# Kernel tuning notes

Hardware: AMD Instinct MI355X
Metric: run time of the kernel (lower is better)

The kernel has to match this reference:

```python
import jax, jax.numpy as jnp
import numpy as np

INF = jnp.inf

def _pairwise_dist(x, y):
    # torch.cdist(x, y, p=2): Euclidean distance matrix [B, N, M]
    x2 = jnp.sum(x * x, axis=-1)  # [B, N]
    y2 = jnp.sum(y * y, axis=-1)  # [B, M]
    sq = x2[:, :, None] + y2[:, None, :] - 2.0 * jnp.einsum('bnf,bmf->bnm', x, y)
    return jnp.sqrt(jnp.maximum(sq, 0.0))

def _dtw_distance(x, y):
    # Anti-diagonal (wavefront) formulation of the DTW DP recurrence:
    # D[i,j] = dist[i,j] + min(D[i-1,j], D[i,j-1], D[i-1,j-1]), D[0,0] = dist[0,0]
    B, N, _ = x.shape
    M = y.shape[1]
    dist = _pairwise_dist(x, y)  # [B, N, M]
    iarr = jnp.arange(N)

    def shift(a):  # prepend inf along the i axis (access index i-1)
        return jnp.concatenate([jnp.full((B, 1), INF, a.dtype), a[:, :-1]], axis=1)

    def step(carry, d):
        prev1, prev2 = carry  # diagonals d-1 and d-2, each [B, N]; prev1[i] = D[i, d-1-i]
        j = d - iarr
        valid = (j >= 0) & (j < M)
        jcl = jnp.clip(j, 0, M - 1)
        dist_d = jnp.where(valid[None, :], dist[:, iarr, jcl], INF)  # dist[i, d-i]
        cand = jnp.minimum(prev1, jnp.minimum(shift(prev1), shift(prev2)))
        # D[0,0] has no predecessors: boundary cell dtw_matrix[0,0] = 0
        cand = jnp.where(((d == 0) & (iarr == 0))[None, :], 0.0, cand)
        cur = jnp.where(valid[None, :], dist_d + cand, INF)
        return (cur, prev1), None

    init = (jnp.full((B, N), INF, dist.dtype), jnp.full((B, N), INF, dist.dtype))
    (last, _), _ = jax.lax.scan(step, init, jnp.arange(N + M - 1))
    return last[:, N - 1]  # D[N-1, M-1] per batch element

def setup_inputs() -> dict:
    key = jax.random.key(0)
    kx, ky = jax.random.split(key)
    B, N, M, F = 8, 2048, 2048, 64
    x = jax.random.normal(kx, (B, N, F), dtype=jnp.float32)
    y = jax.random.normal(ky, (B, M, F), dtype=jnp.float32)
    return {"x": x, "y": y}

def reference(x, y):
    # FastDTW(radius=1, normalize=False) batched forward: DTW distances [B]
    return _dtw_distance(x, y)
```

## Files before the change

kernel.cpp:

```cpp
#include <hip/hip_runtime.h>
#include <hip/hip_bf16.h>

#define BB 8
#define NN 2048
#define MM 2048
#define FF 64
#define INF __builtin_inff()

#define STRIPES 1152
#define BANDBYTES (STRIPES * 1024)
#define NBANDS 8
#define DIST_BYTES ((size_t)BB * NBANDS * BANDBYTES)
#define RING_SLOTS 1152
#define RING_BYTES ((size_t)BB * NBANDS * RING_SLOTS * 8)
#define SENT 0x7FC00000u

typedef __hip_bfloat16 bf16;
typedef float f32x2 __attribute__((ext_vector_type(2)));
typedef float f32x4 __attribute__((ext_vector_type(4)));

__device__ __forceinline__ unsigned pk_bf16x2(float a, float b) {
  union { __hip_bfloat162 h; unsigned u; } cv;
  cv.h.x = __float2bfloat16(a);
  cv.h.y = __float2bfloat16(b);
  return cv.u;
}

__device__ __forceinline__ f32x4 mkf4(float a, float b, float c, float d) {
  f32x4 v; v.x = a; v.y = b; v.z = c; v.w = d; return v;
}

__global__ void norms_k(const float* __restrict__ a, float* __restrict__ o, int rows) {
  int r = blockIdx.x * 256 + threadIdx.x;
  if (r >= rows) return;
  const float4* p = (const float4*)(a + (size_t)r * FF);
  float s = 0.f;
#pragma unroll
  for (int q = 0; q < FF / 4; ++q) {
    float4 v = p[q];
    s = fmaf(v.x, v.x, fmaf(v.y, v.y, fmaf(v.z, v.z, fmaf(v.w, v.w, s))));
  }
  o[r] = s;
}

__global__ void fill_k(uint4* __restrict__ p, int n4, unsigned pat) {
  int i = blockIdx.x * 256 + threadIdx.x;
  const int stride = gridDim.x * 256;
  const uint4 v = make_uint4(pat, pat, pat, pat);
  for (; i < n4; i += stride) p[i] = v;
}

__global__ __launch_bounds__(256) void dist_k(const float* __restrict__ X,
                                              const float* __restrict__ Y,
                                              const float* __restrict__ x2,
                                              const float* __restrict__ y2,
                                              char* __restrict__ dist) {
  __shared__ float xs[64][68];
  __shared__ float ysT[64][68];
  const int b = blockIdx.z, i0 = blockIdx.y * 64, j0 = blockIdx.x * 64;
  const int tid = threadIdx.x, tx = tid & 15, ty = tid >> 4;
  const float* Xb = X + ((size_t)b * NN + i0) * FF;
  const float* Yb = Y + ((size_t)b * MM + j0) * FF;
#pragma unroll
  for (int rep = 0; rep < 4; ++rep) {
    int row = rep * 16 + ty;
    float4 vx = *(const float4*)(Xb + row * FF + tx * 4);
    *(float4*)&xs[row][tx * 4] = vx;
    float4 vy = *(const float4*)(Yb + row * FF + tx * 4);
    ysT[tx * 4 + 0][row] = vy.x;
    ysT[tx * 4 + 1][row] = vy.y;
    ysT[tx * 4 + 2][row] = vy.z;
    ysT[tx * 4 + 3][row] = vy.w;
  }
  __syncthreads();

  const int il0 = ty * 4, jl0 = tx * 4;
  float c[4][4] = {};
#pragma unroll
  for (int k = 0; k < FF; ++k) {
    float a0 = xs[il0 + 0][k], a1 = xs[il0 + 1][k], a2 = xs[il0 + 2][k], a3 = xs[il0 + 3][k];
    float4 bv = *(const float4*)&ysT[k][jl0];
    c[0][0] = fmaf(a0, bv.x, c[0][0]); c[0][1] = fmaf(a0, bv.y, c[0][1]);
    c[0][2] = fmaf(a0, bv.z, c[0][2]); c[0][3] = fmaf(a0, bv.w, c[0][3]);
    c[1][0] = fmaf(a1, bv.x, c[1][0]); c[1][1] = fmaf(a1, bv.y, c[1][1]);
    c[1][2] = fmaf(a1, bv.z, c[1][2]); c[1][3] = fmaf(a1, bv.w, c[1][3]);
    c[2][0] = fmaf(a2, bv.x, c[2][0]); c[2][1] = fmaf(a2, bv.y, c[2][1]);
    c[2][2] = fmaf(a2, bv.z, c[2][2]); c[2][3] = fmaf(a2, bv.w, c[2][3]);
    c[3][0] = fmaf(a3, bv.x, c[3][0]); c[3][1] = fmaf(a3, bv.y, c[3][1]);
    c[3][2] = fmaf(a3, bv.z, c[3][2]); c[3][3] = fmaf(a3, bv.w, c[3][3]);
  }

  float x2v[4], y2v[4];
#pragma unroll
  for (int p = 0; p < 4; ++p) x2v[p] = x2[b * NN + i0 + il0 + p];
#pragma unroll
  for (int q = 0; q < 4; ++q) y2v[q] = y2[b * MM + j0 + jl0 + q];
  __syncthreads();
#pragma unroll
  for (int p = 0; p < 4; ++p) {
    float4 r;
    r.x = sqrtf(fmaxf(x2v[p] + y2v[0] - 2.f * c[p][0], 0.f));
    r.y = sqrtf(fmaxf(x2v[p] + y2v[1] - 2.f * c[p][1], 0.f));
    r.z = sqrtf(fmaxf(x2v[p] + y2v[2] - 2.f * c[p][2], 0.f));
    r.w = sqrtf(fmaxf(x2v[p] + y2v[3] - 2.f * c[p][3], 0.f));
    *(float4*)&xs[il0 + p][jl0] = r;
  }
  __syncthreads();

  const int lt = tid & 15, cpp0 = tid >> 4;
  const int l0 = (i0 & 255) >> 2;
  char* bb = dist + (size_t)(b * NBANDS + (i0 >> 8)) * BANDBYTES;
#pragma unroll
  for (int u = 0; u < 4; ++u) {
    int cpp = cpp0 + u * 16;
    int cp = cpp >> 1, par = cpp & 1;
    int l = l0 + lt;
    int t = (j0 >> 1) + cp + 2 * l;
    unsigned w0 = pk_bf16x2(xs[lt * 4 + 0][cpp], xs[lt * 4 + 1][cpp]);
    unsigned w1 = pk_bf16x2(xs[lt * 4 + 2][cpp], xs[lt * 4 + 3][cpp]);
    *(uint2*)(bb + (size_t)t * 1024 + l * 16 + par * 8) = make_uint2(w0, w1);
  }
}


#define TICK(S, QV)                                                     \
  {                                                                     \
    float nAn = __shfl_up(prevA3, 1, 64);        \
    float nBn = __shfl_up(prevB3, 1, 64);                               \
    float rA = __shfl(rvx, (S), 64);                                    \
    float rB = __shfl(rvy, (S), 64);                                    \
    float upA = isl0 ? rA : nA;                                         \
    float upB = isl0 ? rB : nB;                                         \
    float dgA = isl0 ? topPrev : nBp;                                   \
    float dA0 = __uint_as_float((QV).x << 16);                          \
    float dA1 = __uint_as_float((QV).x & 0xFFFF0000u);                  \
    float dA2 = __uint_as_float((QV).y << 16);                          \
    float dA3 = __uint_as_float((QV).y & 0xFFFF0000u);                  \
    float dB0 = __uint_as_float((QV).z << 16);                          \
    float dB1 = __uint_as_float((QV).z & 0xFFFF0000u);                  \
    float dB2 = __uint_as_float((QV).w << 16);                          \
    float dB3 = __uint_as_float((QV).w & 0xFFFF0000u);                  \
    float A0 = dA0 + fminf(fminf(P0, dgA), upA);                        \
    float A1 = dA1 + fminf(fminf(P1, P0), A0);                          \
    float A2 = dA2 + fminf(fminf(P2, P1), A1);                          \
    float A3 = dA3 + fminf(fminf(P3, P2), A2);                          \
    float B0 = dB0 + fminf(fminf(A0, upA), upB);                        \
    float B1 = dB1 + fminf(fminf(A1, A0), B0);                          \
    float B2 = dB2 + fminf(fminf(A2, A1), B1);                          \
    float B3 = dB3 + fminf(fminf(A3, A2), B2);                          \
    P0 = B0; P1 = B1; P2 = B2; P3 = B3;                                 \
    prevA3 = A3; prevB3 = B3;                                           \
    nBp = nB; nA = nAn; nB = nBn;                                       \
    topPrev = rB;                                                       \
    pubA[S] = A3; pubB[S] = B3;                                         \
  }

#define LDA4(A, B, C, D, BASE)                                          \
  asm volatile("global_load_dwordx4 %0, %4, off\n\t"                    \
               "global_load_dwordx4 %1, %4, off offset:1024\n\t"        \
               "global_load_dwordx4 %2, %4, off offset:2048\n\t"        \
               "global_load_dwordx4 %3, %4, off offset:3072"            \
               : "=&v"(A), "=&v"(B), "=&v"(C), "=&v"(D)                 \
               : "v"(BASE)                                              \
               : "memory")

#define LOADQA(DST, CB)                                                 \
  {                                                                     \
    const char* qn_ = bandbase + ((size_t)(CB) << 14) + (lane << 4);    \
    LDA4(DST[0], DST[1], DST[2], DST[3], qn_);                          \
    LDA4(DST[4], DST[5], DST[6], DST[7], qn_ + 4096);                   \
    LDA4(DST[8], DST[9], DST[10], DST[11], qn_ + 8192);                 \
    LDA4(DST[12], DST[13], DST[14], DST[15], qn_ + 12288);              \
  }

#define RINGADDR(CB) (ringIn + ((((size_t)(CB) << 4) + 126 + (lane & 15)) << 3))

#define RINGLOAD(RV, CB)                                                \
  asm volatile("global_load_dwordx2 %0, %1, off sc0 sc1"                \
               : "=&v"(RV) : "v"(RINGADDR(CB)) : "memory")

#define VERIFY(RV, CB)                                                  \
  if (g && (CB) <= 63) {                                                \
    while (__float_as_uint((RV).x) == SENT) {                           \
      __builtin_amdgcn_s_sleep(4);                                      \
      asm volatile("global_load_dwordx2 %0, %1, off sc0 sc1\n\t"        \
                   "s_waitcnt vmcnt(0)"                                 \
                   : "=&v"(RV) : "v"(RINGADDR(CB)) : "memory");         \
    }                                                                   \
  }

#define PUBLISH(CP)                                                     \
  if (lane == 63) {                                                     \
    char* rp_ = (char*)ringOut + ((size_t)(CP) << 7);                   \
    f32x4 f0 = mkf4(pubA[0], pubB[0], pubA[1], pubB[1]);                \
    f32x4 f1 = mkf4(pubA[2], pubB[2], pubA[3], pubB[3]);                \
    f32x4 f2 = mkf4(pubA[4], pubB[4], pubA[5], pubB[5]);                \
    f32x4 f3 = mkf4(pubA[6], pubB[6], pubA[7], pubB[7]);                \
    f32x4 f4 = mkf4(pubA[8], pubB[8], pubA[9], pubB[9]);                \
    f32x4 f5 = mkf4(pubA[10], pubB[10], pubA[11], pubB[11]);            \
    f32x4 f6 = mkf4(pubA[12], pubB[12], pubA[13], pubB[13]);            \
    f32x4 f7 = mkf4(pubA[14], pubB[14], pubA[15], pubB[15]);            \
    asm volatile(                                                       \
        "global_store_dwordx4 %8, %0, off sc0 sc1\n\t"                  \
        "global_store_dwordx4 %8, %1, off offset:16 sc0 sc1\n\t"        \
        "global_store_dwordx4 %8, %2, off offset:32 sc0 sc1\n\t"        \
        "global_store_dwordx4 %8, %3, off offset:48 sc0 sc1\n\t"        \
        "global_store_dwordx4 %8, %4, off offset:64 sc0 sc1\n\t"        \
        "global_store_dwordx4 %8, %5, off offset:80 sc0 sc1\n\t"        \
        "global_store_dwordx4 %8, %6, off offset:96 sc0 sc1\n\t"        \
        "global_store_dwordx4 %8, %7, off offset:112 sc0 sc1"           \
        :: "v"(f0), "v"(f1), "v"(f2), "v"(f3), "v"(f4), "v"(f5),        \
           "v"(f6), "v"(f7), "v"(rp_)                                   \
        : "memory");                                                    \
  }

#define CHUNK(CUR, NXT, RVC, RVN, CC)                                   \
  do {                                                                  \
    const int c_ = (CC);                                                \
    asm volatile("s_waitcnt vmcnt(0)" ::: "memory");                    \
    __builtin_amdgcn_sched_barrier(0);                                  \
    VERIFY(RVC, c_);                                                    \
    float rvx = RVC.x, rvy = RVC.y;                                     \
    if (g && c_ + 1 <= 63) { RINGLOAD(RVN, c_ + 1); }                   \
    else { RVN.x = INF; RVN.y = INF; }                                  \
    LOADQA(NXT, (c_ < 71 ? c_ + 1 : 71));                               \
    if (c_ > 0) PUBLISH(c_ - 1);                                        \
    __builtin_amdgcn_sched_barrier(0);                                  \
    TICK(0, CUR[0])  TICK(1, CUR[1])  TICK(2, CUR[2])  TICK(3, CUR[3])  \
    TICK(4, CUR[4])  TICK(5, CUR[5])  TICK(6, CUR[6])  TICK(7, CUR[7])  \
    TICK(8, CUR[8])  TICK(9, CUR[9])  TICK(10, CUR[10]) TICK(11, CUR[11]) \
    TICK(12, CUR[12]) TICK(13, CUR[13]) TICK(14, CUR[14]) TICK(15, CUR[15]) \
  } while (0)

__global__ __launch_bounds__(64, 1) void dp_k(const char* __restrict__ dist,
                                              float2* __restrict__ ring,
                                              float* __restrict__ out) {
  const int bid = blockIdx.x;
  const int g = bid & 7, b = bid >> 3;
  const int lane = threadIdx.x;
  const bool isl0 = (lane == 0);
  const char* bandbase = dist + (size_t)bid * BANDBYTES;
  float2* ringOut = ring + (size_t)bid * RING_SLOTS;
  const char* ringIn = (const char*)(ring + (size_t)(bid - 1) * RING_SLOTS);

  float P0 = INF, P1 = INF, P2 = INF, P3 = INF;
  float prevA3 = INF, prevB3 = INF;
  float nA = INF, nB = INF, nBp = INF;
  float topPrev = (g == 0 && lane == 0) ? 0.f : INF;
  float pubA[16], pubB[16];
  uint4 qa[16], qb[16];
  f32x2 rva, rvb;
  rva.x = INF; rva.y = INF; rvb.x = INF; rvb.y = INF;

  LOADQA(qa, 0);
  if (g) RINGLOAD(rva, 0);

  for (int cc = 0; cc < 72; cc += 2) {
    CHUNK(qa, qb, rva, rvb, cc);
    CHUNK(qb, qa, rvb, rva, cc + 1);
  }
  PUBLISH(71);

  if (g == 7 && lane == 63) out[b] = pubB[13];
}

extern "C" void kernel_launch(void* const* d_in, const int* in_sizes, int n_in,
                              void* d_out, int out_size, void* d_ws, size_t ws_size,
                              hipStream_t stream) {
  const float* X = (const float*)d_in[0];
  const float* Y = (const float*)d_in[1];
  float* out = (float*)d_out;

  float* x2 = (float*)d_ws;
  float* y2 = x2 + BB * NN;
  char* dist = (char*)d_ws + 131072;
  float2* ring = (float2*)(dist + DIST_BYTES);

  norms_k<<<dim3((BB * NN + 255) / 256), dim3(256), 0, stream>>>(X, x2, BB * NN);
  norms_k<<<dim3((BB * MM + 255) / 256), dim3(256), 0, stream>>>(Y, y2, BB * MM);
  fill_k<<<dim3(2048), dim3(256), 0, stream>>>((uint4*)dist, (int)(DIST_BYTES / 16), 0x7F7F7F7Fu);
  fill_k<<<dim3(144), dim3(256), 0, stream>>>((uint4*)ring, (int)(RING_BYTES / 16), SENT);

  dist_k<<<dim3(MM / 64, NN / 64, BB), dim3(256), 0, stream>>>(X, Y, x2, y2, dist);
  dp_k<<<dim3(BB * NBANDS), dim3(64), 0, stream>>>(dist, ring, out);
}
```

Before: 320.5 us.

## Fill only pad stripes, relax DP wait count, prefetch ring shuffles

The full-buffer fill of the skewed distance layout is replaced by a fill that writes only the stripes outside the region dist_k writes (the first 126 and those from 1024 on), which cuts a large memset. The DP loop now waits with vmcnt(8) instead of draining all outstanding memory operations, so publish stores can overlap the next chunk. The ring-value shuffles are also software-pipelined one tick ahead. This relies on the vmcnt ordering and on the fill pattern covering exactly the cells dist_k never writes, so a wrong count could read stale data.

```diff
diff --git a/kernel.cpp b/kernel.cpp
--- a/kernel.cpp
+++ b/kernel.cpp
@@ -25,7 +25,6 @@
   cv.h.y = __float2bfloat16(b);
   return cv.u;
 }
-
 __device__ __forceinline__ f32x4 mkf4(float a, float b, float c, float d) {
   f32x4 v; v.x = a; v.y = b; v.z = c; v.w = d; return v;
 }
@@ -48,6 +47,15 @@
   const int stride = gridDim.x * 256;
   const uint4 v = make_uint4(pat, pat, pat, pat);
   for (; i < n4; i += stride) p[i] = v;
+}
+
+__global__ void fill2_k(char* __restrict__ dist) {
+  int i = blockIdx.x * 256 + threadIdx.x;
+  int band = i / 16256, rem = i - band * 16256;
+  int stripe = rem >> 6, word = rem & 63;
+  int t = stripe < 126 ? stripe : 1024 + (stripe - 126);
+  uint4* p = (uint4*)(dist + (size_t)band * BANDBYTES + (size_t)t * 1024 + word * 16);
+  *p = make_uint4(0x7F7F7F7Fu, 0x7F7F7F7Fu, 0x7F7F7F7Fu, 0x7F7F7F7Fu);
 }
 
 __global__ __launch_bounds__(256) void dist_k(const float* __restrict__ X,
@@ -123,14 +131,17 @@
 }
 
 
-#define TICK(S, QV)                                                     \
+#define TICK(S, QV, DONEXT)                                             \
   {                                                                     \
-    float nAn = __shfl_up(prevA3, 1, 64);        \
+    float nAn = __shfl_up(prevA3, 1, 64);                               \
     float nBn = __shfl_up(prevB3, 1, 64);                               \
-    float rA = __shfl(rvx, (S), 64);                                    \
-    float rB = __shfl(rvy, (S), 64);                                    \
-    float upA = isl0 ? rA : nA;                                         \
-    float upB = isl0 ? rB : nB;                                         \
+    float rAn = 0.f, rBn = 0.f;                                         \
+    if (DONEXT) {                                                       \
+      rAn = __shfl(rvx, (S) + 1, 64);                                   \
+      rBn = __shfl(rvy, (S) + 1, 64);                                   \
+    }                                                                   \
+    float upA = isl0 ? rAc : nA;                                        \
+    float upB = isl0 ? rBc : nB;                                        \
     float dgA = isl0 ? topPrev : nBp;                                   \
     float dA0 = __uint_as_float((QV).x << 16);                          \
     float dA1 = __uint_as_float((QV).x & 0xFFFF0000u);                  \
@@ -151,7 +162,8 @@
     P0 = B0; P1 = B1; P2 = B2; P3 = B3;                                 \
     prevA3 = A3; prevB3 = B3;                                           \
     nBp = nB; nA = nAn; nB = nBn;                                       \
-    topPrev = rB;                                                       \
+    topPrev = rBc;                                                      \
+    if (DONEXT) { rAc = rAn; rBc = rBn; }                               \
     pubA[S] = A3; pubB[S] = B3;                                         \
   }
 
@@ -217,19 +229,24 @@
 #define CHUNK(CUR, NXT, RVC, RVN, CC)                                   \
   do {                                                                  \
     const int c_ = (CC);                                                \
-    asm volatile("s_waitcnt vmcnt(0)" ::: "memory");                    \
+    if (c_ == 1) { asm volatile("s_waitcnt vmcnt(0)" ::: "memory"); }   \
+    else         { asm volatile("s_waitcnt vmcnt(8)" ::: "memory"); }   \
     __builtin_amdgcn_sched_barrier(0);                                  \
     VERIFY(RVC, c_);                                                    \
     float rvx = RVC.x, rvy = RVC.y;                                     \
+    rAc = __shfl(rvx, 0, 64);                                           \
+    rBc = __shfl(rvy, 0, 64);                                           \
     if (g && c_ + 1 <= 63) { RINGLOAD(RVN, c_ + 1); }                   \
     else { RVN.x = INF; RVN.y = INF; }                                  \
     LOADQA(NXT, (c_ < 71 ? c_ + 1 : 71));                               \
     if (c_ > 0) PUBLISH(c_ - 1);                                        \
     __builtin_amdgcn_sched_barrier(0);                                  \
-    TICK(0, CUR[0])  TICK(1, CUR[1])  TICK(2, CUR[2])  TICK(3, CUR[3])  \
-    TICK(4, CUR[4])  TICK(5, CUR[5])  TICK(6, CUR[6])  TICK(7, CUR[7])  \
-    TICK(8, CUR[8])  TICK(9, CUR[9])  TICK(10, CUR[10]) TICK(11, CUR[11]) \
-    TICK(12, CUR[12]) TICK(13, CUR[13]) TICK(14, CUR[14]) TICK(15, CUR[15]) \
+    TICK(0, CUR[0], 1)   TICK(1, CUR[1], 1)   TICK(2, CUR[2], 1)        \
+    TICK(3, CUR[3], 1)   TICK(4, CUR[4], 1)   TICK(5, CUR[5], 1)        \
+    TICK(6, CUR[6], 1)   TICK(7, CUR[7], 1)   TICK(8, CUR[8], 1)        \
+    TICK(9, CUR[9], 1)   TICK(10, CUR[10], 1) TICK(11, CUR[11], 1)      \
+    TICK(12, CUR[12], 1) TICK(13, CUR[13], 1) TICK(14, CUR[14], 1)      \
+    TICK(15, CUR[15], 0)                                                \
   } while (0)
 
 __global__ __launch_bounds__(64, 1) void dp_k(const char* __restrict__ dist,
@@ -246,6 +263,7 @@
   float P0 = INF, P1 = INF, P2 = INF, P3 = INF;
   float prevA3 = INF, prevB3 = INF;
   float nA = INF, nB = INF, nBp = INF;
+  float rAc = INF, rBc = INF;
   float topPrev = (g == 0 && lane == 0) ? 0.f : INF;
   float pubA[16], pubB[16];
   uint4 qa[16], qb[16];
@@ -253,7 +271,9 @@
   rva.x = INF; rva.y = INF; rvb.x = INF; rvb.y = INF;
 
   LOADQA(qa, 0);
-  if (g) RINGLOAD(rva, 0);
+  if (g) { RINGLOAD(rva, 0); }
+  asm volatile("s_waitcnt vmcnt(0)" ::: "memory");
+  __builtin_amdgcn_sched_barrier(0);
 
   for (int cc = 0; cc < 72; cc += 2) {
     CHUNK(qa, qb, rva, rvb, cc);
@@ -278,7 +298,7 @@
 
   norms_k<<<dim3((BB * NN + 255) / 256), dim3(256), 0, stream>>>(X, x2, BB * NN);
   norms_k<<<dim3((BB * MM + 255) / 256), dim3(256), 0, stream>>>(Y, y2, BB * MM);
-  fill_k<<<dim3(2048), dim3(256), 0, stream>>>((uint4*)dist, (int)(DIST_BYTES / 16), 0x7F7F7F7Fu);
+  fill2_k<<<dim3(4064), dim3(256), 0, stream>>>(dist);
   fill_k<<<dim3(144), dim3(256), 0, stream>>>((uint4*)ring, (int)(RING_BYTES / 16), SENT);
 
   dist_k<<<dim3(MM / 64, NN / 64, BB), dim3(256), 0, stream>>>(X, Y, x2, y2, dist);
```

New measurement: 286.5 us. 1.12x faster.
